# Performance work log

Measured on AMD Instinct MI355X. Metric: run time of the kernel, lower is better.

The kernel has to match this reference:

```python
import jax, jax.numpy as jnp
import numpy as np

GAMMA = 1.0          # softmin temperature (module default gamma=1.0)
BIG = 1e30           # finite stand-in for +inf (avoids NaN grads through masked cells)
# step_sizes = [[1,0],[0,1],[1,1]], global_step_weights = [1,1,1], normalization='N'

B, N, M, D = 64, 512, 512, 128


def setup_inputs() -> dict:
    key = jax.random.key(0)
    k1, k2 = jax.random.split(key)
    X = jax.random.normal(k1, (B, N, D), dtype=jnp.float32)
    Y = jax.random.normal(k2, (B, M, D), dtype=jnp.float32)
    return {"X": X, "Y": Y}


def _mse_cost(X, Y):
    # C[b,n,m] = mean_d (X[b,n,d] - Y[b,m,d])^2, expanded to avoid a BxNxMxD intermediate
    d = X.shape[-1]
    x2 = jnp.sum(X * X, axis=-1)                      # (B, N)
    y2 = jnp.sum(Y * Y, axis=-1)                      # (B, M)
    xy = jnp.einsum('bnd,bmd->bnm', X, Y)             # (B, N, M)
    return (x2[:, :, None] + y2[:, None, :] - 2.0 * xy) / d


def _soft_dtw(C):
    # Soft-DTW DP via anti-diagonal wavefront scan.
    # R[n,m] = softmin_gamma(R[n-1,m]+c, R[n,m-1]+c, R[n-1,m-1]+c), R[0,0]=C[0,0]
    # (all global step weights are 1.0). Returns R[N-1, M-1] per batch element.
    b, n, m = C.shape
    i_idx = jnp.arange(n)
    ds = jnp.arange(n + m - 1)
    cols = ds[:, None] - i_idx[None, :]               # (n+m-1, n): col index on each diagonal
    valid = (cols >= 0) & (cols < m)
    colsc = jnp.clip(cols, 0, m - 1)
    Cs = C[:, i_idx[None, :], colsc]                  # (b, n+m-1, n) skewed cost
    Cs = jnp.where(valid[None], Cs, 0.0)
    Cs = jnp.transpose(Cs, (1, 0, 2))                 # (n+m-1, b, n)

    pad = jnp.full((b, 1), BIG, C.dtype)

    def shift(r):  # access index i-1 along the diagonal
        return jnp.concatenate([pad, r[:, :-1]], axis=1)

    def step(carry, inp):
        prev, prev2 = carry                           # diagonals d-1, d-2: (b, n)
        c, val, d = inp
        # candidates: steps (1,0), (0,1), (1,1)
        a = jnp.stack([shift(prev) + c, prev + c, shift(prev2) + c], axis=0)  # (3, b, n)
        mn = jax.lax.stop_gradient(jnp.min(a, axis=0))
        r = mn - GAMMA * jnp.log(jnp.sum(jnp.exp((mn - a) / GAMMA), axis=0))
        # start boundary condition (0,0) with W_start=1
        r = jnp.where((d == 0) & (i_idx[None, :] == 0), c, r)
        r = jnp.where(val[None, :], r, BIG)
        return (r, prev), None

    init = (jnp.full((b, n), BIG, C.dtype), jnp.full((b, n), BIG, C.dtype))
    (last, _), _ = jax.lax.scan(step, init, (Cs, valid, ds))
    # end boundary (N-1, M-1) with additive W_end=0
    return last[:, n - 1]


def reference(X, Y):
    C = _mse_cost(X, Y)
    cost = _soft_dtw(C)                               # (B,)
    # normalization='N': mean over batch of cost / N
    return jnp.mean(cost / X.shape[1])
```

## Files before the change

kernel.cpp:

```cpp
#include <hip/hip_runtime.h>
#include <math.h>

#define BATCH 64
#define NN 512
#define MM 512
#define DD 128
#define BIGF 1e30f
#define KLOG2E 1.442695040888963f
#define LN2F   0.693147180559945f
#define BIGK   (BIGF * KLOG2E)

#define NA 768
#define NP 256

typedef __attribute__((ext_vector_type(2))) float f32x2;
typedef __attribute__((ext_vector_type(4))) float f32x4;
typedef __attribute__((ext_vector_type(8))) short s16x8;

__device__ __forceinline__ unsigned short f2bf(float f) {
    unsigned u = __float_as_uint(f);
    u += 0x7FFFu + ((u >> 16) & 1u);
    return (unsigned short)(u >> 16);
}

#define LSI(A, IP) ((A) * 32 + ((IP) ^ ((A) & 31)))

__global__ __launch_bounds__(256) void cost_diag_mfma(const float* __restrict__ X,
                                                      const float* __restrict__ Y,
                                                      f32x2* __restrict__ Cd) {
    __shared__ alignas(16) short smem[2 * 64 * 128];
    __shared__ float x2s[64];
    __shared__ float y2s[64];
    short* Xbf = smem;
    short* Ybf = smem + 64 * 128;
    f32x2* Ls  = (f32x2*)smem;

    int b  = blockIdx.z;
    int ti = blockIdx.y * 64;
    int tj = blockIdx.x * 64;
    int t  = threadIdx.x;
    int l  = t & 63;
    int w  = t >> 6;

    const float* Xb = X + ((size_t)b * NN + ti) * DD;
    const float* Yb = Y + ((size_t)b * MM + tj) * DD;

    int rw  = t >> 4;
    int k8l = t & 15;
    float xs_acc[4], ys_acc[4];
    #pragma unroll
    for (int it = 0; it < 4; ++it) {
        int r = rw + it * 16;
        const float* sx = Xb + (size_t)r * DD + k8l * 8;
        const float* sy = Yb + (size_t)r * DD + k8l * 8;
        float4 x0 = *(const float4*)sx;
        float4 x1 = *(const float4*)(sx + 4);
        float4 y0 = *(const float4*)sy;
        float4 y1 = *(const float4*)(sy + 4);
        xs_acc[it] = x0.x*x0.x + x0.y*x0.y + x0.z*x0.z + x0.w*x0.w
                   + x1.x*x1.x + x1.y*x1.y + x1.z*x1.z + x1.w*x1.w;
        ys_acc[it] = y0.x*y0.x + y0.y*y0.y + y0.z*y0.z + y0.w*y0.w
                   + y1.x*y1.x + y1.y*y1.y + y1.z*y1.z + y1.w*y1.w;
        s16x8 xv, yv;
        xv[0] = (short)f2bf(x0.x); xv[1] = (short)f2bf(x0.y);
        xv[2] = (short)f2bf(x0.z); xv[3] = (short)f2bf(x0.w);
        xv[4] = (short)f2bf(x1.x); xv[5] = (short)f2bf(x1.y);
        xv[6] = (short)f2bf(x1.z); xv[7] = (short)f2bf(x1.w);
        yv[0] = (short)f2bf(y0.x); yv[1] = (short)f2bf(y0.y);
        yv[2] = (short)f2bf(y0.z); yv[3] = (short)f2bf(y0.w);
        yv[4] = (short)f2bf(y1.x); yv[5] = (short)f2bf(y1.y);
        yv[6] = (short)f2bf(y1.z); yv[7] = (short)f2bf(y1.w);
        int sw = (r * 16 + (k8l ^ (r & 7))) * 8;
        *(s16x8*)&Xbf[sw] = xv;
        *(s16x8*)&Ybf[sw] = yv;
    }
    #pragma unroll
    for (int it = 0; it < 4; ++it) {
        float xs = xs_acc[it], ys = ys_acc[it];
        #pragma unroll
        for (int m = 8; m >= 1; m >>= 1) {
            xs += __shfl_xor(xs, m, 16);
            ys += __shfl_xor(ys, m, 16);
        }
        if (k8l == 0) { x2s[rw + it * 16] = xs; y2s[rw + it * 16] = ys; }
    }
    __syncthreads();

    f32x4 acc0 = {0.f,0.f,0.f,0.f}, acc1 = acc0, acc2 = acc0, acc3 = acc0;
    int ar = 16 * w + (l & 15);
    int kb = l >> 4;
    int c0 = l & 15;
    #pragma unroll
    for (int kk = 0; kk < 4; ++kk) {
        int k8 = kk * 4 + kb;
        s16x8 af = *(const s16x8*)&Xbf[(ar * 16 + (k8 ^ (ar & 7))) * 8];
        s16x8 b0 = *(const s16x8*)&Ybf[((c0     ) * 16 + (k8 ^ ((c0     ) & 7))) * 8];
        s16x8 b1 = *(const s16x8*)&Ybf[((c0 + 16) * 16 + (k8 ^ ((c0 + 16) & 7))) * 8];
        s16x8 b2 = *(const s16x8*)&Ybf[((c0 + 32) * 16 + (k8 ^ ((c0 + 32) & 7))) * 8];
        s16x8 b3 = *(const s16x8*)&Ybf[((c0 + 48) * 16 + (k8 ^ ((c0 + 48) & 7))) * 8];
        acc0 = __builtin_amdgcn_mfma_f32_16x16x32_bf16(af, b0, acc0, 0, 0, 0);
        acc1 = __builtin_amdgcn_mfma_f32_16x16x32_bf16(af, b1, acc1, 0, 0, 0);
        acc2 = __builtin_amdgcn_mfma_f32_16x16x32_bf16(af, b2, acc2, 0, 0, 0);
        acc3 = __builtin_amdgcn_mfma_f32_16x16x32_bf16(af, b3, acc3, 0, 0, 0);
    }

    const float inv = KLOG2E / (float)DD;
    int i0l = 16 * w + (l >> 4) * 4;
    float4 xx = *(const float4*)&x2s[i0l];
    float yy0 = y2s[c0];
    float yy1 = y2s[16 + c0];
    float yy2 = y2s[32 + c0];
    float yy3 = y2s[48 + c0];

    __syncthreads();

    int ipl0 = i0l >> 1;
    #define WRT(ACC, YY, C) do {                                               \
        int jl = 16 * (C) + c0;                                                \
        float v0 = (xx.x + (YY) - 2.0f * (ACC)[0]) * inv;                      \
        float v1 = (xx.y + (YY) - 2.0f * (ACC)[1]) * inv;                      \
        float v2 = (xx.z + (YY) - 2.0f * (ACC)[2]) * inv;                      \
        float v3 = (xx.w + (YY) - 2.0f * (ACC)[3]) * inv;                      \
        Ls[LSI(ipl0 + jl, ipl0)]         = f32x2{v0, v1};                      \
        Ls[LSI(ipl0 + 1 + jl, ipl0 + 1)] = f32x2{v2, v3};                      \
    } while (0)
    WRT(acc0, yy0, 0); WRT(acc1, yy1, 1); WRT(acc2, yy2, 2); WRT(acc3, yy3, 3);
    #undef WRT
    __syncthreads();

    f32x2* Cdb = Cd + (size_t)b * (NA * NP);
    int base_a = (ti >> 1) + tj;
    int ipbase = (ti >> 1);
    #pragma unroll
    for (int k = 0; k < 12; ++k) {
        int f  = t + k * 256;
        int al = f >> 5;
        int il = f & 31;
        int d  = al - il;
        if ((unsigned)d < 64u)
            Cdb[(size_t)(base_a + al) * NP + ipbase + il] = Ls[LSI(al, il)];
    }
}

#define RING 8
#define KCH 16
#define ESK 15
#define NITER 51

__global__ __launch_bounds__(256) void sdtw_diag_kernel(const f32x2* __restrict__ Cd,
                                                        float* __restrict__ part) {
    int b = blockIdx.x;
    int p = threadIdx.x;
    int l = p & 63;
    int w = p >> 6;
    int wm1 = (w == 0) ? 0 : (w - 1);
    int wsk = ESK * w;
    int off = p + wsk;
    const char* CbL = (const char*)Cd + (size_t)b * (NA * NP * 8) + p * 8;

    __shared__ alignas(16) f32x2 buf[2][4][KCH];

    if (p < 128) ((f32x2*)buf)[p] = f32x2{BIGK, 1.0f};
    __syncthreads();

    float ps0 = BIGK, pq0 = 1.0f;
    float ps1 = BIGK, pq1 = 1.0f;
    float nbc_s = BIGK, nbc_q = 1.0f;
    float nbp_s = BIGK, nbp_q = 1.0f;
    f32x2 carry = {BIGK, 1.0f};
    float qfl = 1.0f;
    float eS = 0.f, lS = 0.f, dS = 0.f, fS = 0.f, gS = 0.f, hS = 0.f;

    f32x2 b0, b1, b2, b3, b4, b5, b6, b7, b8, b9, b10, b11, b12, b13, b14, b15;
    b0=b1=b2=b3=b4=b5=b6=b7=b8=b9=b10=b11=b12=b13=b14=b15 = f32x2{BIGK, 1.0f};

    f32x2 r0, r1, r2, r3, r4, r5, r6, r7;

#define LOADPD(REG, AV) do {                                                   \
    int a_ = (AV);                                                             \
    a_ = a_ < 0 ? 0 : (a_ > NA - 1 ? NA - 1 : a_);                             \
    const char* pa_ = CbL + (unsigned)a_ * (NP * 8u);                          \
    asm volatile("global_load_dwordx2 %0, %1, off"                             \
                 : "=&v"(REG) : "v"(pa_) : "memory");                          \
} while (0)

    LOADPD(r0, 0 - wsk); LOADPD(r1, 1 - wsk); LOADPD(r2, 2 - wsk);
    LOADPD(r3, 3 - wsk); LOADPD(r4, 4 - wsk); LOADPD(r5, 5 - wsk);
    LOADPD(r6, 6 - wsk); LOADPD(r7, 7 - wsk);

#define SCHAIN(CC, S_, SUX, SDX) do {                                          \
    float su_, sd_;                                                            \
    if (l == 0) {                                                              \
        if (w == 0) { su_ = BIGK; sd_ = ((S_) == 0) ? 0.0f : BIGK; }           \
        else        { su_ = (SUX); sd_ = (SDX); }                              \
    } else { su_ = nbc_s; sd_ = nbp_s; }                                       \
    if ((unsigned)j_ < 512u) {                                                 \
        float lAs = ps0;                                                       \
        float m1;                                                              \
        asm("v_min3_f32 %0, %1, %2, %3" : "=v"(m1) : "v"(su_), "v"(lAs), "v"(sd_)); \
        asm("v_exp_f32 %0, %1" : "=v"(eS) : "v"(m1 - su_));                    \
        asm("v_exp_f32 %0, %1" : "=v"(lS) : "v"(m1 - lAs));                    \
        asm("v_exp_f32 %0, %1" : "=v"(dS) : "v"(m1 - sd_));                    \
        float sA = (CC).x + m1;                                                \
        float m2;                                                              \
        asm("v_min3_f32 %0, %1, %2, %3" : "=v"(m2) : "v"(sA), "v"(ps1), "v"(lAs)); \
        asm("v_exp_f32 %0, %1" : "=v"(fS) : "v"(m2 - sA));                     \
        asm("v_exp_f32 %0, %1" : "=v"(gS) : "v"(m2 - ps1));                    \
        asm("v_exp_f32 %0, %1" : "=v"(hS) : "v"(m2 - lAs));                    \
        ps0 = sA;                                                              \
        ps1 = (CC).y + m2;                                                     \
    }                                                                          \
} while (0)

#define QRESOLVE(JR, QUY, QDY) do {                                            \
    float qu_, qd_;                                                            \
    if (l == 0) {                                                              \
        if (w == 0) { qu_ = 1.0f; qd_ = 1.0f; }                                \
        else        { qu_ = (QUY); qd_ = (QDY); }                              \
    } else { qu_ = nbc_q; qd_ = nbp_q; }                                       \
    if ((unsigned)(JR) < 512u) {                                               \
        float qAo = pq0;                                                       \
        float qA = __builtin_fmaf(qu_, eS, __builtin_fmaf(pq0, lS, qd_ * dS)); \
        float qB = __builtin_fmaf(qA, fS, __builtin_fmaf(pq1, gS, qAo * hS));  \
        pq0 = qA; pq1 = qB;                                                    \
    }                                                                          \
} while (0)

#define STEPN(REG, SIG, BSS, BSQ, SUX, SDX, QUY, QDY) do {                     \
    int s_ = sbase + (SIG);                                                    \
    int j_ = s_ - off;                                                         \
    f32x2 cc;                                                                  \
    asm volatile("s_waitcnt vmcnt(7)" : "=v"(cc) : "0"(REG));                  \
    QRESOLVE(j_ - 1, QUY, QDY);                                                \
    BSQ.y = pq1;                                                               \
    SCHAIN(cc, s_, SUX, SDX);                                                  \
    BSS.x = ps1;                                                               \
    float shs_, shq_;                                                          \
    asm("v_mov_b32_dpp %0, %2 wave_shr:1 row_mask:0xf bank_mask:0xf\n\t"       \
        "v_mov_b32_dpp %1, %3 wave_shr:1 row_mask:0xf bank_mask:0xf"           \
        : "=v"(shs_), "=v"(shq_) : "v"(ps1), "v"(pq1));                        \
    nbp_s = nbc_s; nbc_s = shs_;                                               \
    nbp_q = nbc_q; nbc_q = shq_;                                               \
    LOADPD(REG, s_ + RING - wsk);                                              \
} while (0)

#define STEP0(REG, BSS) do {                                                   \
    int s_ = sbase;                                                            \
    int j_ = s_ - off;                                                         \
    f32x2 cc;                                                                  \
    asm volatile("s_waitcnt vmcnt(7)" : "=v"(cc) : "0"(REG));                  \
    SCHAIN(cc, s_, c0[0], carry.x);                                            \
    BSS.x = ps1;                                                               \
    float shs_;                                                                \
    asm("v_mov_b32_dpp %0, %1 wave_shr:1 row_mask:0xf bank_mask:0xf"           \
        : "=v"(shs_) : "v"(ps1));                                              \
    nbp_s = nbc_s; nbc_s = shs_;                                               \
    nbp_q = nbc_q; nbc_q = qfl;                                                \
    LOADPD(REG, s_ + RING - wsk);                                              \
} while (0)

#define FLUSHQ() do {                                                          \
    int jr_ = sbase + 15 - off;                                                \
    QRESOLVE(jr_, c7[3], c7[1]);                                               \
    b15.y = pq1;                                                               \
    asm("v_mov_b32_dpp %0, %1 wave_shr:1 row_mask:0xf bank_mask:0xf"           \
        : "=v"(qfl) : "v"(pq1));                                               \
} while (0)

#define RENORMD(S, Q) do {                                                     \
    int e_ = (__float_as_int(Q) >> 23) - 127;                                  \
    Q = __int_as_float(__float_as_int(Q) - (e_ << 23));                        \
    S = S - (float)e_;                                                         \
} while (0)

    for (int I = 0; I < NITER; ++I) {
        asm volatile("s_waitcnt lgkmcnt(0)" ::: "memory");
        __builtin_amdgcn_s_barrier();
        asm volatile("" ::: "memory");
        const f32x4* rq = (const f32x4*)&buf[(I + 1) & 1][wm1][0];
        f32x4 c0 = rq[0], c1 = rq[1], c2 = rq[2], c3 = rq[3];
        f32x4 c4 = rq[4], c5 = rq[5], c6 = rq[6], c7 = rq[7];
        int sbase = I * KCH;
        STEP0(r0, b0);
        STEPN(r1, 1,  b1,  b0,  c0[2], c0[0], c0[1], carry.y);
        STEPN(r2, 2,  b2,  b1,  c1[0], c0[2], c0[3], c0[1]);
        STEPN(r3, 3,  b3,  b2,  c1[2], c1[0], c1[1], c0[3]);
        STEPN(r4, 4,  b4,  b3,  c2[0], c1[2], c1[3], c1[1]);
        STEPN(r5, 5,  b5,  b4,  c2[2], c2[0], c2[1], c1[3]);
        STEPN(r6, 6,  b6,  b5,  c3[0], c2[2], c2[3], c2[1]);
        STEPN(r7, 7,  b7,  b6,  c3[2], c3[0], c3[1], c2[3]);
        STEPN(r0, 8,  b8,  b7,  c4[0], c3[2], c3[3], c3[1]);
        STEPN(r1, 9,  b9,  b8,  c4[2], c4[0], c4[1], c3[3]);
        STEPN(r2, 10, b10, b9,  c5[0], c4[2], c4[3], c4[1]);
        STEPN(r3, 11, b11, b10, c5[2], c5[0], c5[1], c4[3]);
        STEPN(r4, 12, b12, b11, c6[0], c5[2], c5[3], c5[1]);
        STEPN(r5, 13, b13, b12, c6[2], c6[0], c6[1], c5[3]);
        STEPN(r6, 14, b14, b13, c7[0], c6[2], c6[3], c6[1]);
        STEPN(r7, 15, b15, b14, c7[2], c7[0], c7[1], c6[3]);
        FLUSHQ();
        carry = f32x2{c7[2], c7[3]};
        if (l == 63) {
            f32x2* wbp = &buf[I & 1][w][0];
            wbp[0]  = b0;  wbp[1]  = b1;  wbp[2]  = b2;  wbp[3]  = b3;
            wbp[4]  = b4;  wbp[5]  = b5;  wbp[6]  = b6;  wbp[7]  = b7;
            wbp[8]  = b8;  wbp[9]  = b9;  wbp[10] = b10; wbp[11] = b11;
            wbp[12] = b12; wbp[13] = b13; wbp[14] = b14; wbp[15] = b15;
        }
        RENORMD(ps0, pq0);
        RENORMD(ps1, pq1);
    }

    if (p == 255) {
        float lg;
        asm("v_log_f32 %0, %1" : "=v"(lg) : "v"(pq1));
        part[b] = (ps1 - lg) * LN2F;
    }
#undef STEPN
#undef STEP0
#undef FLUSHQ
#undef QRESOLVE
#undef SCHAIN
#undef LOADPD
#undef RENORMD
}

__global__ __launch_bounds__(64) void reduce_kernel(const float* __restrict__ part,
                                                    float* __restrict__ out) {
    int l = threadIdx.x;
    float v = part[l];
    #pragma unroll
    for (int m = 32; m >= 1; m >>= 1) v += __shfl_xor(v, m, 64);
    if (l == 0) out[0] = v / (float)(BATCH * NN);
}

extern "C" void kernel_launch(void* const* d_in, const int* in_sizes, int n_in,
                              void* d_out, int out_size, void* d_ws, size_t ws_size,
                              hipStream_t stream) {
    const float* X = (const float*)d_in[0];
    const float* Y = (const float*)d_in[1];
    float* out = (float*)d_out;
    char* ws = (char*)d_ws;

    const size_t cdBytes = (size_t)BATCH * NA * NP * 8;

    f32x2* Cd   = (f32x2*)ws;
    float* part = (float*)(ws + cdBytes);

    dim3 g(MM / 64, NN / 64, BATCH);
    cost_diag_mfma<<<g, 256, 0, stream>>>(X, Y, Cd);

    sdtw_diag_kernel<<<BATCH, 256, 0, stream>>>(Cd, part);

    reduce_kernel<<<1, 64, 0, stream>>>(part, out);
}
```

Before: 145.5 us.

## Give each DP thread four rows instead of two and halve the wavefront block

The soft-DTW wavefront now assigns four consecutive rows to each thread, not two. The skewed cost layout is repacked into float4 quads (640 diagonals by 128 quads), and the DP kernel runs with 128 threads across two waves. This cuts the skew latency so the loop needs fewer outer iterations, and it halves the cross-wave shared-memory handoff. In exchange each thread carries a longer serial dependency chain per diagonal, with 12 exps per step, and fewer waves are available to hide latency.

```diff
diff --git a/kernel.cpp b/kernel.cpp
--- a/kernel.cpp
+++ b/kernel.cpp
@@ -10,8 +10,8 @@
 #define LN2F   0.693147180559945f
 #define BIGK   (BIGF * KLOG2E)
 
-#define NA 768
-#define NP 256
+#define NA4 640
+#define NP4 128
 
 typedef __attribute__((ext_vector_type(2))) float f32x2;
 typedef __attribute__((ext_vector_type(4))) float f32x4;
@@ -23,17 +23,17 @@
     return (unsigned short)(u >> 16);
 }
 
-#define LSI(A, IP) ((A) * 32 + ((IP) ^ ((A) & 31)))
+#define LSI4(A, IQ) ((A) * 16 + ((IQ) ^ ((A) & 15)))
 
 __global__ __launch_bounds__(256) void cost_diag_mfma(const float* __restrict__ X,
                                                       const float* __restrict__ Y,
-                                                      f32x2* __restrict__ Cd) {
+                                                      f32x4* __restrict__ Cd) {
     __shared__ alignas(16) short smem[2 * 64 * 128];
     __shared__ float x2s[64];
     __shared__ float y2s[64];
     short* Xbf = smem;
     short* Ybf = smem + 64 * 128;
-    f32x2* Ls  = (f32x2*)smem;
+    f32x4* Ls4 = (f32x4*)smem;
 
     int b  = blockIdx.z;
     int ti = blockIdx.y * 64;
@@ -114,79 +114,93 @@
 
     __syncthreads();
 
-    int ipl0 = i0l >> 1;
+    int iql = i0l >> 2;
     #define WRT(ACC, YY, C) do {                                               \
         int jl = 16 * (C) + c0;                                                \
-        float v0 = (xx.x + (YY) - 2.0f * (ACC)[0]) * inv;                      \
-        float v1 = (xx.y + (YY) - 2.0f * (ACC)[1]) * inv;                      \
-        float v2 = (xx.z + (YY) - 2.0f * (ACC)[2]) * inv;                      \
-        float v3 = (xx.w + (YY) - 2.0f * (ACC)[3]) * inv;                      \
-        Ls[LSI(ipl0 + jl, ipl0)]         = f32x2{v0, v1};                      \
-        Ls[LSI(ipl0 + 1 + jl, ipl0 + 1)] = f32x2{v2, v3};                      \
+        f32x4 v;                                                               \
+        v[0] = (xx.x + (YY) - 2.0f * (ACC)[0]) * inv;                          \
+        v[1] = (xx.y + (YY) - 2.0f * (ACC)[1]) * inv;                          \
+        v[2] = (xx.z + (YY) - 2.0f * (ACC)[2]) * inv;                          \
+        v[3] = (xx.w + (YY) - 2.0f * (ACC)[3]) * inv;                          \
+        Ls4[LSI4(iql + jl, iql)] = v;                                          \
     } while (0)
     WRT(acc0, yy0, 0); WRT(acc1, yy1, 1); WRT(acc2, yy2, 2); WRT(acc3, yy3, 3);
     #undef WRT
     __syncthreads();
 
-    f32x2* Cdb = Cd + (size_t)b * (NA * NP);
-    int base_a = (ti >> 1) + tj;
-    int ipbase = (ti >> 1);
-    #pragma unroll
-    for (int k = 0; k < 12; ++k) {
+    f32x4* Cdb = Cd + (size_t)b * (NA4 * NP4);
+    int base_a = (ti >> 2) + tj;
+    int iqbase = ti >> 2;
+    #pragma unroll
+    for (int k = 0; k < 5; ++k) {
         int f  = t + k * 256;
-        int al = f >> 5;
-        int il = f & 31;
-        int d  = al - il;
-        if ((unsigned)d < 64u)
-            Cdb[(size_t)(base_a + al) * NP + ipbase + il] = Ls[LSI(al, il)];
+        int al = f >> 4;
+        int il = f & 15;
+        if (al < 79 && (unsigned)(al - il) < 64u)
+            Cdb[(size_t)(base_a + al) * NP4 + iqbase + il] = Ls4[LSI4(al, il)];
     }
 }
 
 #define RING 8
 #define KCH 16
 #define ESK 15
-#define NITER 51
-
-__global__ __launch_bounds__(256) void sdtw_diag_kernel(const f32x2* __restrict__ Cd,
+#define NITER 41
+
+__global__ __launch_bounds__(128) void sdtw_diag_kernel(const f32x4* __restrict__ Cd,
                                                         float* __restrict__ part) {
     int b = blockIdx.x;
     int p = threadIdx.x;
     int l = p & 63;
     int w = p >> 6;
-    int wm1 = (w == 0) ? 0 : (w - 1);
     int wsk = ESK * w;
     int off = p + wsk;
-    const char* CbL = (const char*)Cd + (size_t)b * (NA * NP * 8) + p * 8;
-
-    __shared__ alignas(16) f32x2 buf[2][4][KCH];
-
-    if (p < 128) ((f32x2*)buf)[p] = f32x2{BIGK, 1.0f};
+    const char* CbL = (const char*)Cd + (size_t)b * (NA4 * NP4 * 16) + p * 16;
+
+    __shared__ alignas(16) f32x2 buf[2][KCH];
+
+    if (p < 32) ((f32x2*)buf)[p] = f32x2{BIGK, 1.0f};
     __syncthreads();
 
-    float ps0 = BIGK, pq0 = 1.0f;
-    float ps1 = BIGK, pq1 = 1.0f;
-    float nbc_s = BIGK, nbc_q = 1.0f;
-    float nbp_s = BIGK, nbp_q = 1.0f;
+    float ps0 = BIGK, ps1 = BIGK, ps2 = BIGK, ps3 = BIGK;
+    float pq0 = 1.0f, pq1 = 1.0f, pq2 = 1.0f, pq3 = 1.0f;
+    float nbc_s = BIGK, nbp_s = BIGK;
+    float nbc_q = 1.0f, nbp_q = 1.0f;
     f32x2 carry = {BIGK, 1.0f};
     float qfl = 1.0f;
-    float eS = 0.f, lS = 0.f, dS = 0.f, fS = 0.f, gS = 0.f, hS = 0.f;
+    float eu0=0,el0=0,ed0=0, eu1=0,el1=0,ed1=0;
+    float eu2=0,el2=0,ed2=0, eu3=0,el3=0,ed3=0;
 
     f32x2 b0, b1, b2, b3, b4, b5, b6, b7, b8, b9, b10, b11, b12, b13, b14, b15;
     b0=b1=b2=b3=b4=b5=b6=b7=b8=b9=b10=b11=b12=b13=b14=b15 = f32x2{BIGK, 1.0f};
 
-    f32x2 r0, r1, r2, r3, r4, r5, r6, r7;
+    f32x4 rq0, rq1, rq2, rq3, rq4, rq5, rq6, rq7;
 
 #define LOADPD(REG, AV) do {                                                   \
     int a_ = (AV);                                                             \
-    a_ = a_ < 0 ? 0 : (a_ > NA - 1 ? NA - 1 : a_);                             \
-    const char* pa_ = CbL + (unsigned)a_ * (NP * 8u);                          \
-    asm volatile("global_load_dwordx2 %0, %1, off"                             \
+    a_ = a_ < 0 ? 0 : (a_ > NA4 - 1 ? NA4 - 1 : a_);                           \
+    const char* pa_ = CbL + (unsigned)a_ * (NP4 * 16u);                        \
+    asm volatile("global_load_dwordx4 %0, %1, off"                             \
                  : "=&v"(REG) : "v"(pa_) : "memory");                          \
 } while (0)
 
-    LOADPD(r0, 0 - wsk); LOADPD(r1, 1 - wsk); LOADPD(r2, 2 - wsk);
-    LOADPD(r3, 3 - wsk); LOADPD(r4, 4 - wsk); LOADPD(r5, 5 - wsk);
-    LOADPD(r6, 6 - wsk); LOADPD(r7, 7 - wsk);
+    LOADPD(rq0, 0 - wsk); LOADPD(rq1, 1 - wsk); LOADPD(rq2, 2 - wsk);
+    LOADPD(rq3, 3 - wsk); LOADPD(rq4, 4 - wsk); LOADPD(rq5, 5 - wsk);
+    LOADPD(rq6, 6 - wsk); LOADPD(rq7, 7 - wsk);
+
+#define QRES(JR, QUY, QDY) do {                                                \
+    float qu_, qd_;                                                            \
+    if (l == 0) {                                                              \
+        if (w == 0) { qu_ = 1.0f; qd_ = 1.0f; }                                \
+        else        { qu_ = (QUY); qd_ = (QDY); }                              \
+    } else { qu_ = nbc_q; qd_ = nbp_q; }                                       \
+    if ((unsigned)(JR) < 512u) {                                               \
+        float o0 = pq0, o1 = pq1, o2 = pq2;                                    \
+        pq0 = __builtin_fmaf(qu_, eu0, __builtin_fmaf(pq0, el0, qd_ * ed0));   \
+        pq1 = __builtin_fmaf(pq0, eu1, __builtin_fmaf(pq1, el1, o0 * ed1));    \
+        pq2 = __builtin_fmaf(pq1, eu2, __builtin_fmaf(pq2, el2, o1 * ed2));    \
+        pq3 = __builtin_fmaf(pq2, eu3, __builtin_fmaf(pq3, el3, o2 * ed3));    \
+    }                                                                          \
+} while (0)
 
 #define SCHAIN(CC, S_, SUX, SDX) do {                                          \
     float su_, sd_;                                                            \
@@ -195,65 +209,62 @@
         else        { su_ = (SUX); sd_ = (SDX); }                              \
     } else { su_ = nbc_s; sd_ = nbp_s; }                                       \
     if ((unsigned)j_ < 512u) {                                                 \
-        float lAs = ps0;                                                       \
+        float m0;                                                              \
+        asm("v_min3_f32 %0, %1, %2, %3" : "=v"(m0) : "v"(su_), "v"(ps0), "v"(sd_)); \
+        asm("v_exp_f32 %0, %1" : "=v"(eu0) : "v"(m0 - su_));                   \
+        asm("v_exp_f32 %0, %1" : "=v"(el0) : "v"(m0 - ps0));                   \
+        asm("v_exp_f32 %0, %1" : "=v"(ed0) : "v"(m0 - sd_));                   \
+        float sA0 = (CC)[0] + m0;                                              \
         float m1;                                                              \
-        asm("v_min3_f32 %0, %1, %2, %3" : "=v"(m1) : "v"(su_), "v"(lAs), "v"(sd_)); \
-        asm("v_exp_f32 %0, %1" : "=v"(eS) : "v"(m1 - su_));                    \
-        asm("v_exp_f32 %0, %1" : "=v"(lS) : "v"(m1 - lAs));                    \
-        asm("v_exp_f32 %0, %1" : "=v"(dS) : "v"(m1 - sd_));                    \
-        float sA = (CC).x + m1;                                                \
+        asm("v_min3_f32 %0, %1, %2, %3" : "=v"(m1) : "v"(sA0), "v"(ps1), "v"(ps0)); \
+        asm("v_exp_f32 %0, %1" : "=v"(eu1) : "v"(m1 - sA0));                   \
+        asm("v_exp_f32 %0, %1" : "=v"(el1) : "v"(m1 - ps1));                   \
+        asm("v_exp_f32 %0, %1" : "=v"(ed1) : "v"(m1 - ps0));                   \
+        float sA1 = (CC)[1] + m1;                                              \
         float m2;                                                              \
-        asm("v_min3_f32 %0, %1, %2, %3" : "=v"(m2) : "v"(sA), "v"(ps1), "v"(lAs)); \
-        asm("v_exp_f32 %0, %1" : "=v"(fS) : "v"(m2 - sA));                     \
-        asm("v_exp_f32 %0, %1" : "=v"(gS) : "v"(m2 - ps1));                    \
-        asm("v_exp_f32 %0, %1" : "=v"(hS) : "v"(m2 - lAs));                    \
-        ps0 = sA;                                                              \
-        ps1 = (CC).y + m2;                                                     \
+        asm("v_min3_f32 %0, %1, %2, %3" : "=v"(m2) : "v"(sA1), "v"(ps2), "v"(ps1)); \
+        asm("v_exp_f32 %0, %1" : "=v"(eu2) : "v"(m2 - sA1));                   \
+        asm("v_exp_f32 %0, %1" : "=v"(el2) : "v"(m2 - ps2));                   \
+        asm("v_exp_f32 %0, %1" : "=v"(ed2) : "v"(m2 - ps1));                   \
+        float sA2 = (CC)[2] + m2;                                              \
+        float m3;                                                              \
+        asm("v_min3_f32 %0, %1, %2, %3" : "=v"(m3) : "v"(sA2), "v"(ps3), "v"(ps2)); \
+        asm("v_exp_f32 %0, %1" : "=v"(eu3) : "v"(m3 - sA2));                   \
+        asm("v_exp_f32 %0, %1" : "=v"(el3) : "v"(m3 - ps3));                   \
+        asm("v_exp_f32 %0, %1" : "=v"(ed3) : "v"(m3 - ps2));                   \
+        float sA3 = (CC)[3] + m3;                                              \
+        ps0 = sA0; ps1 = sA1; ps2 = sA2; ps3 = sA3;                            \
     }                                                                          \
 } while (0)
 
-#define QRESOLVE(JR, QUY, QDY) do {                                            \
-    float qu_, qd_;                                                            \
-    if (l == 0) {                                                              \
-        if (w == 0) { qu_ = 1.0f; qd_ = 1.0f; }                                \
-        else        { qu_ = (QUY); qd_ = (QDY); }                              \
-    } else { qu_ = nbc_q; qd_ = nbp_q; }                                       \
-    if ((unsigned)(JR) < 512u) {                                               \
-        float qAo = pq0;                                                       \
-        float qA = __builtin_fmaf(qu_, eS, __builtin_fmaf(pq0, lS, qd_ * dS)); \
-        float qB = __builtin_fmaf(qA, fS, __builtin_fmaf(pq1, gS, qAo * hS));  \
-        pq0 = qA; pq1 = qB;                                                    \
-    }                                                                          \
-} while (0)
-
-#define STEPN(REG, SIG, BSS, BSQ, SUX, SDX, QUY, QDY) do {                     \
+#define STEPD(REG, SIG, BSS, BSQ, SUX, SDX, QUY, QDY) do {                     \
     int s_ = sbase + (SIG);                                                    \
     int j_ = s_ - off;                                                         \
-    f32x2 cc;                                                                  \
+    f32x4 cc;                                                                  \
     asm volatile("s_waitcnt vmcnt(7)" : "=v"(cc) : "0"(REG));                  \
-    QRESOLVE(j_ - 1, QUY, QDY);                                                \
-    BSQ.y = pq1;                                                               \
+    QRES(j_ - 1, QUY, QDY);                                                    \
+    BSQ.y = pq3;                                                               \
     SCHAIN(cc, s_, SUX, SDX);                                                  \
-    BSS.x = ps1;                                                               \
+    BSS.x = ps3;                                                               \
     float shs_, shq_;                                                          \
     asm("v_mov_b32_dpp %0, %2 wave_shr:1 row_mask:0xf bank_mask:0xf\n\t"       \
         "v_mov_b32_dpp %1, %3 wave_shr:1 row_mask:0xf bank_mask:0xf"           \
-        : "=v"(shs_), "=v"(shq_) : "v"(ps1), "v"(pq1));                        \
+        : "=v"(shs_), "=v"(shq_) : "v"(ps3), "v"(pq3));                        \
     nbp_s = nbc_s; nbc_s = shs_;                                               \
     nbp_q = nbc_q; nbc_q = shq_;                                               \
     LOADPD(REG, s_ + RING - wsk);                                              \
 } while (0)
 
-#define STEP0(REG, BSS) do {                                                   \
+#define STEP0D(REG, BSS) do {                                                  \
     int s_ = sbase;                                                            \
     int j_ = s_ - off;                                                         \
-    f32x2 cc;                                                                  \
+    f32x4 cc;                                                                  \
     asm volatile("s_waitcnt vmcnt(7)" : "=v"(cc) : "0"(REG));                  \
     SCHAIN(cc, s_, c0[0], carry.x);                                            \
-    BSS.x = ps1;                                                               \
+    BSS.x = ps3;                                                               \
     float shs_;                                                                \
     asm("v_mov_b32_dpp %0, %1 wave_shr:1 row_mask:0xf bank_mask:0xf"           \
-        : "=v"(shs_) : "v"(ps1));                                              \
+        : "=v"(shs_) : "v"(ps3));                                              \
     nbp_s = nbc_s; nbc_s = shs_;                                               \
     nbp_q = nbc_q; nbc_q = qfl;                                                \
     LOADPD(REG, s_ + RING - wsk);                                              \
@@ -261,10 +272,10 @@
 
 #define FLUSHQ() do {                                                          \
     int jr_ = sbase + 15 - off;                                                \
-    QRESOLVE(jr_, c7[3], c7[1]);                                               \
-    b15.y = pq1;                                                               \
+    QRES(jr_, c7[3], c7[1]);                                                   \
+    b15.y = pq3;                                                               \
     asm("v_mov_b32_dpp %0, %1 wave_shr:1 row_mask:0xf bank_mask:0xf"           \
-        : "=v"(qfl) : "v"(pq1));                                               \
+        : "=v"(qfl) : "v"(pq3));                                               \
 } while (0)
 
 #define RENORMD(S, Q) do {                                                     \
@@ -277,30 +288,30 @@
         asm volatile("s_waitcnt lgkmcnt(0)" ::: "memory");
         __builtin_amdgcn_s_barrier();
         asm volatile("" ::: "memory");
-        const f32x4* rq = (const f32x4*)&buf[(I + 1) & 1][wm1][0];
+        const f32x4* rq = (const f32x4*)&buf[(I + 1) & 1][0];
         f32x4 c0 = rq[0], c1 = rq[1], c2 = rq[2], c3 = rq[3];
         f32x4 c4 = rq[4], c5 = rq[5], c6 = rq[6], c7 = rq[7];
         int sbase = I * KCH;
-        STEP0(r0, b0);
-        STEPN(r1, 1,  b1,  b0,  c0[2], c0[0], c0[1], carry.y);
-        STEPN(r2, 2,  b2,  b1,  c1[0], c0[2], c0[3], c0[1]);
-        STEPN(r3, 3,  b3,  b2,  c1[2], c1[0], c1[1], c0[3]);
-        STEPN(r4, 4,  b4,  b3,  c2[0], c1[2], c1[3], c1[1]);
-        STEPN(r5, 5,  b5,  b4,  c2[2], c2[0], c2[1], c1[3]);
-        STEPN(r6, 6,  b6,  b5,  c3[0], c2[2], c2[3], c2[1]);
-        STEPN(r7, 7,  b7,  b6,  c3[2], c3[0], c3[1], c2[3]);
-        STEPN(r0, 8,  b8,  b7,  c4[0], c3[2], c3[3], c3[1]);
-        STEPN(r1, 9,  b9,  b8,  c4[2], c4[0], c4[1], c3[3]);
-        STEPN(r2, 10, b10, b9,  c5[0], c4[2], c4[3], c4[1]);
-        STEPN(r3, 11, b11, b10, c5[2], c5[0], c5[1], c4[3]);
-        STEPN(r4, 12, b12, b11, c6[0], c5[2], c5[3], c5[1]);
-        STEPN(r5, 13, b13, b12, c6[2], c6[0], c6[1], c5[3]);
-        STEPN(r6, 14, b14, b13, c7[0], c6[2], c6[3], c6[1]);
-        STEPN(r7, 15, b15, b14, c7[2], c7[0], c7[1], c6[3]);
+        STEP0D(rq0, b0);
+        STEPD(rq1, 1,  b1,  b0,  c0[2], c0[0], c0[1], carry.y);
+        STEPD(rq2, 2,  b2,  b1,  c1[0], c0[2], c0[3], c0[1]);
+        STEPD(rq3, 3,  b3,  b2,  c1[2], c1[0], c1[1], c0[3]);
+        STEPD(rq4, 4,  b4,  b3,  c2[0], c1[2], c1[3], c1[1]);
+        STEPD(rq5, 5,  b5,  b4,  c2[2], c2[0], c2[1], c1[3]);
+        STEPD(rq6, 6,  b6,  b5,  c3[0], c2[2], c2[3], c2[1]);
+        STEPD(rq7, 7,  b7,  b6,  c3[2], c3[0], c3[1], c2[3]);
+        STEPD(rq0, 8,  b8,  b7,  c4[0], c3[2], c3[3], c3[1]);
+        STEPD(rq1, 9,  b9,  b8,  c4[2], c4[0], c4[1], c3[3]);
+        STEPD(rq2, 10, b10, b9,  c5[0], c4[2], c4[3], c4[1]);
+        STEPD(rq3, 11, b11, b10, c5[2], c5[0], c5[1], c4[3]);
+        STEPD(rq4, 12, b12, b11, c6[0], c5[2], c5[3], c5[1]);
+        STEPD(rq5, 13, b13, b12, c6[2], c6[0], c6[1], c5[3]);
+        STEPD(rq6, 14, b14, b13, c7[0], c6[2], c6[3], c6[1]);
+        STEPD(rq7, 15, b15, b14, c7[2], c7[0], c7[1], c6[3]);
         FLUSHQ();
         carry = f32x2{c7[2], c7[3]};
-        if (l == 63) {
-            f32x2* wbp = &buf[I & 1][w][0];
+        if (p == 63) {
+            f32x2* wbp = &buf[I & 1][0];
             wbp[0]  = b0;  wbp[1]  = b1;  wbp[2]  = b2;  wbp[3]  = b3;
             wbp[4]  = b4;  wbp[5]  = b5;  wbp[6]  = b6;  wbp[7]  = b7;
             wbp[8]  = b8;  wbp[9]  = b9;  wbp[10] = b10; wbp[11] = b11;
@@ -308,17 +319,19 @@
         }
         RENORMD(ps0, pq0);
         RENORMD(ps1, pq1);
-    }
-
-    if (p == 255) {
+        RENORMD(ps2, pq2);
+        RENORMD(ps3, pq3);
+    }
+
+    if (p == 127) {
         float lg;
-        asm("v_log_f32 %0, %1" : "=v"(lg) : "v"(pq1));
-        part[b] = (ps1 - lg) * LN2F;
-    }
-#undef STEPN
-#undef STEP0
+        asm("v_log_f32 %0, %1" : "=v"(lg) : "v"(pq3));
+        part[b] = (ps3 - lg) * LN2F;
+    }
+#undef STEPD
+#undef STEP0D
 #undef FLUSHQ
-#undef QRESOLVE
+#undef QRES
 #undef SCHAIN
 #undef LOADPD
 #undef RENORMD
@@ -341,15 +354,15 @@
     float* out = (float*)d_out;
     char* ws = (char*)d_ws;
 
-    const size_t cdBytes = (size_t)BATCH * NA * NP * 8;
-
-    f32x2* Cd   = (f32x2*)ws;
+    const size_t cdBytes = (size_t)BATCH * NA4 * NP4 * 16;
+
+    f32x4* Cd   = (f32x4*)ws;
     float* part = (float*)(ws + cdBytes);
 
     dim3 g(MM / 64, NN / 64, BATCH);
     cost_diag_mfma<<<g, 256, 0, stream>>>(X, Y, Cd);
 
-    sdtw_diag_kernel<<<BATCH, 256, 0, stream>>>(Cd, part);
+    sdtw_diag_kernel<<<BATCH, 128, 0, stream>>>(Cd, part);
 
     reduce_kernel<<<1, 64, 0, stream>>>(part, out);
 }
```

After: 164.6 us. +13.2%, slower.

## Store skewed cost matrix as fp16 pairs and fold final reduction into DP kernel

Applied to the files above, without the earlier changes.

The diagonal-skewed cost matrix is now written as packed half2 values instead of float2, halving the workspace traffic between the cost kernel and the wavefront DP kernel. The DP kernel loads single dwords and converts to float on the fly. The separate reduction launch is replaced by a last-block-done atomic counter inside the DP kernel, with the counter reset by the first cost-kernel thread. This saves bandwidth and one launch, at the cost of fp16 rounding of costs, which could affect accuracy over the 1023-step accumulation.

```diff
diff --git a/kernel.cpp b/kernel.cpp
--- a/kernel.cpp
+++ b/kernel.cpp
@@ -1,4 +1,5 @@
 #include <hip/hip_runtime.h>
+#include <hip/hip_fp16.h>
 #include <math.h>
 
 #define BATCH 64
@@ -27,13 +28,14 @@
 
 __global__ __launch_bounds__(256) void cost_diag_mfma(const float* __restrict__ X,
                                                       const float* __restrict__ Y,
-                                                      f32x2* __restrict__ Cd) {
+                                                      unsigned* __restrict__ Cd,
+                                                      unsigned* __restrict__ cnt) {
     __shared__ alignas(16) short smem[2 * 64 * 128];
     __shared__ float x2s[64];
     __shared__ float y2s[64];
     short* Xbf = smem;
     short* Ybf = smem + 64 * 128;
-    f32x2* Ls  = (f32x2*)smem;
+    unsigned* Ls = (unsigned*)smem;
 
     int b  = blockIdx.z;
     int ti = blockIdx.y * 64;
@@ -41,6 +43,8 @@
     int t  = threadIdx.x;
     int l  = t & 63;
     int w  = t >> 6;
+
+    if (b == 0 && ti == 0 && tj == 0 && t == 0) *cnt = 0u;
 
     const float* Xb = X + ((size_t)b * NN + ti) * DD;
     const float* Yb = Y + ((size_t)b * MM + tj) * DD;
@@ -121,14 +125,16 @@
         float v1 = (xx.y + (YY) - 2.0f * (ACC)[1]) * inv;                      \
         float v2 = (xx.z + (YY) - 2.0f * (ACC)[2]) * inv;                      \
         float v3 = (xx.w + (YY) - 2.0f * (ACC)[3]) * inv;                      \
-        Ls[LSI(ipl0 + jl, ipl0)]         = f32x2{v0, v1};                      \
-        Ls[LSI(ipl0 + 1 + jl, ipl0 + 1)] = f32x2{v2, v3};                      \
+        __half2 h01 = __floats2half2_rn(v0, v1);                               \
+        __half2 h23 = __floats2half2_rn(v2, v3);                               \
+        Ls[LSI(ipl0 + jl, ipl0)]         = *(unsigned*)&h01;                   \
+        Ls[LSI(ipl0 + 1 + jl, ipl0 + 1)] = *(unsigned*)&h23;                   \
     } while (0)
     WRT(acc0, yy0, 0); WRT(acc1, yy1, 1); WRT(acc2, yy2, 2); WRT(acc3, yy3, 3);
     #undef WRT
     __syncthreads();
 
-    f32x2* Cdb = Cd + (size_t)b * (NA * NP);
+    unsigned* Cdb = Cd + (size_t)b * (NA * NP);
     int base_a = (ti >> 1) + tj;
     int ipbase = (ti >> 1);
     #pragma unroll
@@ -147,8 +153,10 @@
 #define ESK 15
 #define NITER 51
 
-__global__ __launch_bounds__(256) void sdtw_diag_kernel(const f32x2* __restrict__ Cd,
-                                                        float* __restrict__ part) {
+__global__ __launch_bounds__(256) void sdtw_diag_kernel(const unsigned* __restrict__ Cd,
+                                                        float* __restrict__ part,
+                                                        float* __restrict__ out,
+                                                        unsigned* __restrict__ cnt) {
     int b = blockIdx.x;
     int p = threadIdx.x;
     int l = p & 63;
@@ -156,7 +164,7 @@
     int wm1 = (w == 0) ? 0 : (w - 1);
     int wsk = ESK * w;
     int off = p + wsk;
-    const char* CbL = (const char*)Cd + (size_t)b * (NA * NP * 8) + p * 8;
+    const char* CbL = (const char*)Cd + (size_t)b * (NA * NP * 4) + p * 4;
 
     __shared__ alignas(16) f32x2 buf[2][4][KCH];
 
@@ -174,13 +182,13 @@
     f32x2 b0, b1, b2, b3, b4, b5, b6, b7, b8, b9, b10, b11, b12, b13, b14, b15;
     b0=b1=b2=b3=b4=b5=b6=b7=b8=b9=b10=b11=b12=b13=b14=b15 = f32x2{BIGK, 1.0f};
 
-    f32x2 r0, r1, r2, r3, r4, r5, r6, r7;
+    unsigned r0, r1, r2, r3, r4, r5, r6, r7;
 
 #define LOADPD(REG, AV) do {                                                   \
     int a_ = (AV);                                                             \
     a_ = a_ < 0 ? 0 : (a_ > NA - 1 ? NA - 1 : a_);                             \
-    const char* pa_ = CbL + (unsigned)a_ * (NP * 8u);                          \
-    asm volatile("global_load_dwordx2 %0, %1, off"                             \
+    const char* pa_ = CbL + (unsigned)a_ * (NP * 4u);                          \
+    asm volatile("global_load_dword %0, %1, off"                               \
                  : "=&v"(REG) : "v"(pa_) : "memory");                          \
 } while (0)
 
@@ -229,8 +237,11 @@
 #define STEPN(REG, SIG, BSS, BSQ, SUX, SDX, QUY, QDY) do {                     \
     int s_ = sbase + (SIG);                                                    \
     int j_ = s_ - off;                                                         \
+    unsigned bits_;                                                            \
+    asm volatile("s_waitcnt vmcnt(7)" : "=v"(bits_) : "0"(REG));               \
+    __half2 h_ = *(__half2*)&bits_;                                            \
     f32x2 cc;                                                                  \
-    asm volatile("s_waitcnt vmcnt(7)" : "=v"(cc) : "0"(REG));                  \
+    cc.x = __low2float(h_); cc.y = __high2float(h_);                           \
     QRESOLVE(j_ - 1, QUY, QDY);                                                \
     BSQ.y = pq1;                                                               \
     SCHAIN(cc, s_, SUX, SDX);                                                  \
@@ -247,8 +258,11 @@
 #define STEP0(REG, BSS) do {                                                   \
     int s_ = sbase;                                                            \
     int j_ = s_ - off;                                                         \
+    unsigned bits_;                                                            \
+    asm volatile("s_waitcnt vmcnt(7)" : "=v"(bits_) : "0"(REG));               \
+    __half2 h_ = *(__half2*)&bits_;                                            \
     f32x2 cc;                                                                  \
-    asm volatile("s_waitcnt vmcnt(7)" : "=v"(cc) : "0"(REG));                  \
+    cc.x = __low2float(h_); cc.y = __high2float(h_);                           \
     SCHAIN(cc, s_, c0[0], carry.x);                                            \
     BSS.x = ps1;                                                               \
     float shs_;                                                                \
@@ -314,6 +328,16 @@
         float lg;
         asm("v_log_f32 %0, %1" : "=v"(lg) : "v"(pq1));
         part[b] = (ps1 - lg) * LN2F;
+        __threadfence();
+        unsigned prev = __hip_atomic_fetch_add(cnt, 1u, __ATOMIC_ACQ_REL,
+                                               __HIP_MEMORY_SCOPE_AGENT);
+        if (prev == BATCH - 1u) {
+            const volatile float* vp = part;
+            float s = 0.0f;
+            #pragma unroll
+            for (int i = 0; i < BATCH; ++i) s += vp[i];
+            out[0] = s / (float)(BATCH * NN);
+        }
     }
 #undef STEPN
 #undef STEP0
@@ -324,15 +348,6 @@
 #undef RENORMD
 }
 
-__global__ __launch_bounds__(64) void reduce_kernel(const float* __restrict__ part,
-                                                    float* __restrict__ out) {
-    int l = threadIdx.x;
-    float v = part[l];
-    #pragma unroll
-    for (int m = 32; m >= 1; m >>= 1) v += __shfl_xor(v, m, 64);
-    if (l == 0) out[0] = v / (float)(BATCH * NN);
-}
-
 extern "C" void kernel_launch(void* const* d_in, const int* in_sizes, int n_in,
                               void* d_out, int out_size, void* d_ws, size_t ws_size,
                               hipStream_t stream) {
@@ -341,15 +356,14 @@
     float* out = (float*)d_out;
     char* ws = (char*)d_ws;
 
-    const size_t cdBytes = (size_t)BATCH * NA * NP * 8;
-
-    f32x2* Cd   = (f32x2*)ws;
-    float* part = (float*)(ws + cdBytes);
+    const size_t cdBytes = (size_t)BATCH * NA * NP * 4;
+
+    unsigned* Cd   = (unsigned*)ws;
+    float*    part = (float*)(ws + cdBytes);
+    unsigned* cnt  = (unsigned*)(ws + cdBytes + 256);
 
     dim3 g(MM / 64, NN / 64, BATCH);
-    cost_diag_mfma<<<g, 256, 0, stream>>>(X, Y, Cd);
-
-    sdtw_diag_kernel<<<BATCH, 256, 0, stream>>>(Cd, part);
-
-    reduce_kernel<<<1, 64, 0, stream>>>(part, out);
+    cost_diag_mfma<<<g, 256, 0, stream>>>(X, Y, Cd, cnt);
+
+    sdtw_diag_kernel<<<BATCH, 256, 0, stream>>>(Cd, part, out, cnt);
 }
```

Result: slower. 150.2 us (+3.2%).
